# Performance work log

Hardware: AMD Instinct MI355X
Metric: run time of the kernel (lower is better)

## Reference

```python
import jax, jax.numpy as jnp
import numpy as np
from functools import reduce

N_QUBITS = 8
DEPTH = 2
DIM = 2 ** N_QUBITS  # state-vector dimension
HIDDEN = 512


def _cnot_chain_np(n):
    # product of CNOT(w, w+1) for w = 0..n-2, wire 0 = most-significant bit (PennyLane order)
    C4 = np.array([[1, 0, 0, 0], [0, 1, 0, 0], [0, 0, 0, 1], [0, 0, 1, 0]], dtype=np.complex64)
    U = np.eye(2 ** n, dtype=np.complex64)
    for w in range(n - 1):
        full = np.kron(np.kron(np.eye(2 ** w, dtype=np.complex64), C4),
                       np.eye(2 ** (n - w - 2), dtype=np.complex64))
        U = full @ U
    return U

CNOT_CHAIN = jnp.asarray(_cnot_chain_np(N_QUBITS))
# PauliZ on wire 0 (MSB): +1 for basis states with MSB=0, -1 otherwise
Z0 = jnp.asarray(np.where(np.arange(DIM) < DIM // 2, 1.0, -1.0).astype(np.float32))


def _rot(p):
    # PennyLane Rot(phi, theta, omega) = RZ(omega) @ RY(theta) @ RZ(phi)
    phi, th, om = p[0], p[1], p[2]
    c = jnp.cos(th / 2).astype(jnp.complex64)
    s = jnp.sin(th / 2).astype(jnp.complex64)
    ep = jnp.exp(-0.5j * (phi + om).astype(jnp.complex64))  # e^{-i(phi+om)/2}
    em = jnp.exp(0.5j * (phi - om).astype(jnp.complex64))   # e^{ i(phi-om)/2}
    m00 = ep * c
    m01 = -em * s
    m10 = jnp.conj(em) * s
    m11 = jnp.conj(ep) * c
    return jnp.stack([jnp.stack([m00, m01]), jnp.stack([m10, m11])])


def _gate_unitary(P):
    # P: (depth, n_qubits, 3). Circuit (after data RX): per layer Rot on every wire, then CNOT chain.
    U = jnp.eye(DIM, dtype=jnp.complex64)
    for l in range(DEPTH):
        layer = reduce(jnp.kron, [_rot(P[l, w]) for w in range(N_QUBITS)])
        U = CNOT_CHAIN @ (layer @ U)
    return U


def _expval(theta, U):
    # RX(theta)|0...0> = cos(t/2)|0..0> - i sin(t/2)|10..0>; then fixed unitary U; <Z_0>
    col0 = U[:, 0]          # U |00...0>
    col1 = U[:, DIM // 2]   # U |10...0>
    a = jnp.cos(theta / 2)[:, None]
    b = jnp.sin(theta / 2)[:, None]
    psi = a * col0[None, :] - 1j * b * col1[None, :]  # (B, DIM)
    return jnp.sum(Z0 * (psi.real ** 2 + psi.imag ** 2), axis=-1)  # (B,)


def setup_inputs() -> dict:
    key = jax.random.key(0)
    ks = jax.random.split(key, 13)
    T, B, D, H, Q = 256, 128, 512, HIDDEN, N_QUBITS
    inp = {"inputs": jax.random.normal(ks[0], (T, B, D), jnp.float32)}
    for i, g in enumerate(["f", "i", "g", "o"]):
        inp[f"W{g}"] = jax.random.normal(ks[1 + 3 * i], (Q, D + H), jnp.float32) * 0.02
        inp[f"b{g}"] = jnp.zeros((Q,), jnp.float32)
        inp[f"P{g}"] = jax.random.normal(ks[3 + 3 * i], (DEPTH, Q, 3), jnp.float32)
    return inp


def reference(inputs, Wf, bf, Pf, Wi, bi, Pi, Wg, bg, Pg, Wo, bo, Po):
    Uf, Ui, Ug, Uo = _gate_unitary(Pf), _gate_unitary(Pi), _gate_unitary(Pg), _gate_unitary(Po)

    def step(carry, x):
        hx, cx = carry
        comb = jnp.concatenate([x, hx], axis=1)  # (B, D+H)
        f = jax.nn.sigmoid(_expval((comb @ Wf.T + bf)[:, 0], Uf))[:, None]
        i = jax.nn.sigmoid(_expval((comb @ Wi.T + bi)[:, 0], Ui))[:, None]
        g = jnp.tanh(_expval((comb @ Wg.T + bg)[:, 0], Ug))[:, None]
        o = jax.nn.sigmoid(_expval((comb @ Wo.T + bo)[:, 0], Uo))[:, None]
        cx = f * cx + i * g
        hx = o * jnp.tanh(cx)
        return (hx, cx), hx

    B = inputs.shape[1]
    init = (jnp.zeros((B, HIDDEN), inputs.dtype), jnp.zeros((B, HIDDEN), inputs.dtype))
    (hx, cx), outputs = jax.lax.scan(step, init, inputs)
    return outputs, hx, cx
```

## Files before the change

kernel.cpp:

```cpp
#include <hip/hip_runtime.h>
#include <math.h>

#define T_STEPS 256
#define BATCH   128
#define DIMD    512
#define NROWS   (T_STEPS * BATCH)
#define PF      16
#define WRITER_BLOCKS 258
#define GEMV_BLOCKS 2048

#define INV2PI  0.15915494309189535f
#define L2E     1.4426950408889634f
#define TWO_L2E 2.8853900817779268f

#define AGENT __HIP_MEMORY_SCOPE_AGENT

#if __has_builtin(__builtin_amdgcn_sinf)
#define HW_SIN(x) __builtin_amdgcn_sinf(x)
#else
__device__ __forceinline__ float HW_SIN(float x) { return __sinf(x * 6.283185307179586f); }
#endif
#if __has_builtin(__builtin_amdgcn_exp2f)
#define EXP2(x) __builtin_amdgcn_exp2f(x)
#else
#define EXP2(x) exp2f(x)
#endif
#if __has_builtin(__builtin_amdgcn_rcpf)
#define RCP(x) __builtin_amdgcn_rcpf(x)
#else
#define RCP(x) (1.0f / (x))
#endif

__device__ __forceinline__ void  st_rlx(float* p, float v) {
    __hip_atomic_store(p, v, __ATOMIC_RELAXED, AGENT);
}
__device__ __forceinline__ void  st_rlx_i(int* p, int v) {
    __hip_atomic_store(p, v, __ATOMIC_RELAXED, AGENT);
}
__device__ __forceinline__ int   ld_rlx_i(const int* p) {
    return __hip_atomic_load(p, __ATOMIC_RELAXED, AGENT);
}
#define VMFENCE() asm volatile("s_waitcnt vmcnt(0)" ::: "memory")
#define CFENCE()  asm volatile("" ::: "memory")

__global__ __launch_bounds__(256) void prep(
    const float* __restrict__ inp,
    const float* __restrict__ Wf, const float* __restrict__ Wi,
    const float* __restrict__ Wg, const float* __restrict__ Wo,
    const float* __restrict__ bfp, const float* __restrict__ bip,
    const float* __restrict__ bgp, const float* __restrict__ bop,
    const float* __restrict__ Pf, const float* __restrict__ Pi,
    const float* __restrict__ Pg, const float* __restrict__ Po,
    float* __restrict__ gc, int* __restrict__ hProg,
    float4* __restrict__ X4)
{
    const int bid  = blockIdx.x;
    const int wv   = threadIdx.x >> 6;
    const int lane = threadIdx.x & 63;

    if (bid == 0) {
        if (threadIdx.x == 0) { hProg[0] = 0; hProg[1] = 0; }
        const int g = wv;
        const float* P = (g == 0) ? Pf : (g == 1) ? Pi : (g == 2) ? Pg : Po;
        const float* W = (g == 0) ? Wf : (g == 1) ? Wi : (g == 2) ? Wg : Wo;

        __shared__ float s0r[4][256], s0i[4][256], s1r[4][256], s1i[4][256];

#pragma unroll
        for (int j = 0; j < 4; ++j) {
            const int k = lane + 64 * j;
            s0r[g][k] = (k == 0)   ? 1.0f : 0.0f;  s0i[g][k] = 0.0f;
            s1r[g][k] = (k == 128) ? 1.0f : 0.0f;  s1i[g][k] = 0.0f;
        }
        __syncthreads();

        for (int l = 0; l < 2; ++l) {
            for (int w = 0; w < 8; ++w) {
                const float phi = P[l * 24 + w * 3 + 0];
                const float th  = P[l * 24 + w * 3 + 1];
                const float om  = P[l * 24 + w * 3 + 2];
                float sh, chh; __sincosf(0.5f * th, &sh, &chh);
                float sp, cp;  __sincosf(0.5f * (phi + om), &sp, &cp);
                float sm, cm;  __sincosf(0.5f * (phi - om), &sm, &cm);
                const float m00r =  cp * chh, m00i = -sp * chh;
                const float m01r = -cm * sh,  m01i = -sm * sh;
                const float m10r =  cm * sh,  m10i = -sm * sh;
                const float m11r =  cp * chh, m11i =  sp * chh;

                const int shift = 7 - w;
                const int mask  = 1 << shift;

                float n0r[4], n0i[4], n1r[4], n1i[4];
#pragma unroll
                for (int j = 0; j < 4; ++j) {
                    const int k  = lane + 64 * j;
                    const int bit = (k >> shift) & 1;
                    const int i0 = k & ~mask, i1 = k | mask;
                    const float a0r = s0r[g][i0], a0i = s0i[g][i0];
                    const float a1r = s0r[g][i1], a1i = s0i[g][i1];
                    const float b0r = s1r[g][i0], b0i = s1i[g][i0];
                    const float b1r = s1r[g][i1], b1i = s1i[g][i1];
                    const float mr0 = bit ? m10r : m00r, mi0 = bit ? m10i : m00i;
                    const float mr1 = bit ? m11r : m01r, mi1 = bit ? m11i : m01i;
                    n0r[j] = mr0 * a0r - mi0 * a0i + mr1 * a1r - mi1 * a1i;
                    n0i[j] = mr0 * a0i + mi0 * a0r + mr1 * a1i + mi1 * a1r;
                    n1r[j] = mr0 * b0r - mi0 * b0i + mr1 * b1r - mi1 * b1i;
                    n1i[j] = mr0 * b0i + mi0 * b0r + mr1 * b1i + mi1 * b1r;
                }
                __syncthreads();
#pragma unroll
                for (int j = 0; j < 4; ++j) {
                    const int k = lane + 64 * j;
                    s0r[g][k] = n0r[j]; s0i[g][k] = n0i[j];
                    s1r[g][k] = n1r[j]; s1i[g][k] = n1i[j];
                }
                __syncthreads();
            }
            float n0r[4], n0i[4], n1r[4], n1i[4];
#pragma unroll
            for (int j = 0; j < 4; ++j) {
                int src = lane + 64 * j;
                for (int w = 6; w >= 0; --w) {
                    const int cb = (src >> (7 - w)) & 1;
                    src ^= cb << (6 - w);
                }
                n0r[j] = s0r[g][src]; n0i[j] = s0i[g][src];
                n1r[j] = s1r[g][src]; n1i[j] = s1i[g][src];
            }
            __syncthreads();
#pragma unroll
            for (int j = 0; j < 4; ++j) {
                const int k = lane + 64 * j;
                s0r[g][k] = n0r[j]; s0i[g][k] = n0i[j];
                s1r[g][k] = n1r[j]; s1i[g][k] = n1i[j];
            }
            __syncthreads();
        }

        float t00 = 0, t11 = 0, t01 = 0;
#pragma unroll
        for (int j = 0; j < 4; ++j) {
            const int k = lane + 64 * j;
            const float z = (k < 128) ? 1.0f : -1.0f;
            t00 += z * (s0r[g][k] * s0r[g][k] + s0i[g][k] * s0i[g][k]);
            t11 += z * (s1r[g][k] * s1r[g][k] + s1i[g][k] * s1i[g][k]);
            t01 += z * (s0i[g][k] * s1r[g][k] - s0r[g][k] * s1i[g][k]);
        }
        float tsw = 0;
#pragma unroll
        for (int j = 0; j < 8; ++j) tsw += W[512 + lane + 64 * j];

        for (int off = 32; off; off >>= 1) {
            t00 += __shfl_xor(t00, off);
            t11 += __shfl_xor(t11, off);
            t01 += __shfl_xor(t01, off);
            tsw += __shfl_xor(tsw, off);
        }
        if (lane == 0) {
            const float A  = 0.5f * (t00 + t11);
            const float Bc = 0.5f * (t00 - t11);
            const float Bs = -t01;
            const float R  = sqrtf(Bc * Bc + Bs * Bs);
            const float ph = atan2f(Bc, Bs) * INV2PI;
            const float sc = (g == 2) ? TWO_L2E : -L2E;
            gc[4 * g + 0] = sc * A;
            gc[4 * g + 1] = sc * R;
            gc[4 * g + 2] = ph;
            gc[4 * g + 3] = tsw * INV2PI;
        }
        return;
    }

    const int rowbase = (bid - 1) * 16 + wv * 4;

    const float4* wfp = (const float4*)Wf;
    const float4* wip = (const float4*)Wi;
    const float4* wgp = (const float4*)Wg;
    const float4* wop = (const float4*)Wo;
    const float4 fa = wfp[lane], fb = wfp[lane + 64];
    const float4 ia = wip[lane], ib = wip[lane + 64];
    const float4 ga = wgp[lane], gb = wgp[lane + 64];
    const float4 oa = wop[lane], ob = wop[lane + 64];

    const float4* xr = (const float4*)(inp + (size_t)rowbase * DIMD);
    float sums[4][4];
#pragma unroll
    for (int r = 0; r < 4; ++r) {
        const float4 xa = xr[r * 128 + lane];
        const float4 xb = xr[r * 128 + lane + 64];
        sums[r][0] = xa.x * fa.x + xa.y * fa.y + xa.z * fa.z + xa.w * fa.w
                   + xb.x * fb.x + xb.y * fb.y + xb.z * fb.z + xb.w * fb.w;
        sums[r][1] = xa.x * ia.x + xa.y * ia.y + xa.z * ia.z + xa.w * ia.w
                   + xb.x * ib.x + xb.y * ib.y + xb.z * ib.z + xb.w * ib.w;
        sums[r][2] = xa.x * ga.x + xa.y * ga.y + xa.z * ga.z + xa.w * ga.w
                   + xb.x * gb.x + xb.y * gb.y + xb.z * gb.z + xb.w * gb.w;
        sums[r][3] = xa.x * oa.x + xa.y * oa.y + xa.z * oa.z + xa.w * oa.w
                   + xb.x * ob.x + xb.y * ob.y + xb.z * ob.z + xb.w * ob.w;
    }
#pragma unroll
    for (int r = 0; r < 4; ++r)
#pragma unroll
        for (int g = 0; g < 4; ++g)
            for (int off = 32; off; off >>= 1)
                sums[r][g] += __shfl_xor(sums[r][g], off);

    if (lane == 0) {
        const float b0f = bfp[0], b0i = bip[0], b0g = bgp[0], b0o = bop[0];
#pragma unroll
        for (int r = 0; r < 4; ++r) {
            X4[rowbase + r] = make_float4((sums[r][0] + b0f) * INV2PI,
                                          (sums[r][1] + b0i) * INV2PI,
                                          (sums[r][2] + b0g) * INV2PI,
                                          (sums[r][3] + b0o) * INV2PI);
        }
    }
}

__global__ __launch_bounds__(256) void scan_write(
    const float4* __restrict__ X4, const float* __restrict__ gc,
    float* __restrict__ Hs, float* __restrict__ cfin,
    float4* __restrict__ out4, int* __restrict__ hProg)
{
    const int bid  = blockIdx.x;
    const int wv   = threadIdx.x >> 6;
    const int lane = threadIdx.x & 63;

    if (bid == 0) {
        if (threadIdx.x >= BATCH) return;
        const int b = threadIdx.x;

        const float Af = gc[0],  Rf = gc[1],  phf = gc[2],  swf = gc[3];
        const float Ai = gc[4],  Ri = gc[5],  phi_ = gc[6], swi = gc[7];
        const float Ag = gc[8],  Rg = gc[9],  phg = gc[10], swg = gc[11];
        const float Ao = gc[12], Ro = gc[13], pho = gc[14], swo = gc[15];

        float4 p[PF];
#pragma unroll
        for (int j = 0; j < PF; ++j) p[j] = X4[j * BATCH + b];

        float c = 0.0f, h = 0.0f;
        for (int tb = 0; tb < T_STEPS; tb += PF) {
#pragma unroll
            for (int j = 0; j < PF; ++j) {
                const int t = tb + j;
                const float4 xv = p[j];
                p[j] = X4[(t + PF) * BATCH + b];

                const float thf = fmaf(h, swf, xv.x + phf);
                const float thi = fmaf(h, swi, xv.y + phi_);
                const float thg = fmaf(h, swg, xv.z + phg);
                const float tho = fmaf(h, swo, xv.w + pho);
                const float Ef = fmaf(Rf, HW_SIN(thf), Af);
                const float Ei = fmaf(Ri, HW_SIN(thi), Ai);
                const float Eg = fmaf(Rg, HW_SIN(thg), Ag);
                const float Eo = fmaf(Ro, HW_SIN(tho), Ao);
                const float fg = RCP(1.0f + EXP2(Ef));
                const float ig = RCP(1.0f + EXP2(Ei));
                const float og = RCP(1.0f + EXP2(Eo));
                const float gg = 1.0f - 2.0f * RCP(EXP2(Eg) + 1.0f);
                c = fmaf(fg, c, ig * gg);
                const float y = RCP(EXP2(c * TWO_L2E) + 1.0f);
                h = fmaf(-2.0f * og, y, og);
                st_rlx(&Hs[t * BATCH + b], h);
            }
            if (tb == T_STEPS - PF) st_rlx(&cfin[b], c);
            if (((tb + PF) & 31) == 0) {
                VMFENCE();
                if (lane == 0) st_rlx_i(&hProg[wv], tb + PF);
            }
        }
        return;
    }

    const int t  = bid - 1;
    const int qd = wv;
    const int pidx = (qd < 2) ? 0 : 1;
    const int need = (t < 256) ? (t + 1) : 256;

    int cur = ld_rlx_i(&hProg[pidx]);
    while (cur < need) {
        int chunks = ((need - cur) >> 4) + 1;
        for (int s = 0; s < chunks; ++s) __builtin_amdgcn_s_sleep(16);
        cur = ld_rlx_i(&hProg[pidx]);
    }
    CFENCE();

    const float* src = (t == 257) ? cfin : (Hs + ((t >= 256 ? 255 : t) * BATCH));
    const float hv = src[qd * 32 + (lane & 31)];

    size_t base = (t < 256) ? ((size_t)t * 16384)
                : (t == 256 ? (size_t)4194304 : (size_t)4210688);
    base += (size_t)qd * 4096;
#pragma unroll 8
    for (int j = 0; j < 64; ++j) {
        const float v = __shfl(hv, j >> 1);
        out4[base + j * 64 + lane] = make_float4(v, v, v, v);
    }
}

extern "C" void kernel_launch(void* const* d_in, const int* in_sizes, int n_in,
                              void* d_out, int out_size, void* d_ws, size_t ws_size,
                              hipStream_t stream)
{
    const float* inp = (const float*)d_in[0];
    const float* Wf  = (const float*)d_in[1];
    const float* bfv = (const float*)d_in[2];
    const float* Pf  = (const float*)d_in[3];
    const float* Wi  = (const float*)d_in[4];
    const float* biv = (const float*)d_in[5];
    const float* Pi  = (const float*)d_in[6];
    const float* Wg  = (const float*)d_in[7];
    const float* bgv = (const float*)d_in[8];
    const float* Pg  = (const float*)d_in[9];
    const float* Wo  = (const float*)d_in[10];
    const float* bov = (const float*)d_in[11];
    const float* Po  = (const float*)d_in[12];

    float4* X4   = (float4*)d_ws;
    float*  Hs   = (float*)(X4 + NROWS + PF * BATCH);
    float*  cfin = Hs + NROWS;
    float*  gc   = cfin + BATCH;
    int*    hProg = (int*)(gc + 16);

    prep<<<1 + GEMV_BLOCKS, 256, 0, stream>>>(inp, Wf, Wi, Wg, Wo,
                                              bfv, biv, bgv, bov,
                                              Pf, Pi, Pg, Po,
                                              gc, hProg, X4);
    scan_write<<<1 + WRITER_BLOCKS, 256, 0, stream>>>(X4, gc, Hs, cfin,
                                                      (float4*)d_out, hProg);
}
```

Baseline: 57.17 us.

## Algebraically fuse LSTM gate math, coarsen progress signaling, use nontemporal output stores

```diff
diff --git a/kernel.cpp b/kernel.cpp
--- a/kernel.cpp
+++ b/kernel.cpp
@@ -14,6 +14,8 @@
 #define TWO_L2E 2.8853900817779268f
 
 #define AGENT __HIP_MEMORY_SCOPE_AGENT
+
+typedef float f32x4 __attribute__((ext_vector_type(4)));
 
 #if __has_builtin(__builtin_amdgcn_sinf)
 #define HW_SIN(x) __builtin_amdgcn_sinf(x)
@@ -216,7 +218,7 @@
     }
 }
 
-__global__ __launch_bounds__(256) void scan_write(
+__global__ __launch_bounds__(256, 1) void scan_write(
     const float4* __restrict__ X4, const float* __restrict__ gc,
     float* __restrict__ Hs, float* __restrict__ cfin,
     float4* __restrict__ out4, int* __restrict__ hProg)
@@ -234,37 +236,47 @@
         const float Ag = gc[8],  Rg = gc[9],  phg = gc[10], swg = gc[11];
         const float Ao = gc[12], Ro = gc[13], pho = gc[14], swo = gc[15];
 
-        float4 p[PF];
-#pragma unroll
-        for (int j = 0; j < PF; ++j) p[j] = X4[j * BATCH + b];
+        float4 p0, p1, p2, p3, p4, p5, p6, p7,
+               p8, p9, p10, p11, p12, p13, p14, p15;
+
+#define LOADP(J, P) { const float4 v_ = X4[(J) * BATCH + b];                 \
+        P = make_float4(v_.x + phf, v_.y + phi_, v_.z + phg, v_.w + pho); }
+        LOADP(0, p0)   LOADP(1, p1)   LOADP(2, p2)   LOADP(3, p3)
+        LOADP(4, p4)   LOADP(5, p5)   LOADP(6, p6)   LOADP(7, p7)
+        LOADP(8, p8)   LOADP(9, p9)   LOADP(10, p10) LOADP(11, p11)
+        LOADP(12, p12) LOADP(13, p13) LOADP(14, p14) LOADP(15, p15)
+#undef LOADP
 
         float c = 0.0f, h = 0.0f;
         for (int tb = 0; tb < T_STEPS; tb += PF) {
-#pragma unroll
-            for (int j = 0; j < PF; ++j) {
-                const int t = tb + j;
-                const float4 xv = p[j];
-                p[j] = X4[(t + PF) * BATCH + b];
-
-                const float thf = fmaf(h, swf, xv.x + phf);
-                const float thi = fmaf(h, swi, xv.y + phi_);
-                const float thg = fmaf(h, swg, xv.z + phg);
-                const float tho = fmaf(h, swo, xv.w + pho);
-                const float Ef = fmaf(Rf, HW_SIN(thf), Af);
-                const float Ei = fmaf(Ri, HW_SIN(thi), Ai);
-                const float Eg = fmaf(Rg, HW_SIN(thg), Ag);
-                const float Eo = fmaf(Ro, HW_SIN(tho), Ao);
-                const float fg = RCP(1.0f + EXP2(Ef));
-                const float ig = RCP(1.0f + EXP2(Ei));
-                const float og = RCP(1.0f + EXP2(Eo));
-                const float gg = 1.0f - 2.0f * RCP(EXP2(Eg) + 1.0f);
-                c = fmaf(fg, c, ig * gg);
-                const float y = RCP(EXP2(c * TWO_L2E) + 1.0f);
-                h = fmaf(-2.0f * og, y, og);
-                st_rlx(&Hs[t * BATCH + b], h);
-            }
+#define STEP(J, P) {                                                         \
+            const float4 xv = P;                                             \
+            { const float4 v_ = X4[(tb + (J) + PF) * BATCH + b];             \
+              P = make_float4(v_.x + phf, v_.y + phi_,                       \
+                              v_.z + phg, v_.w + pho); }                     \
+            const float thf = fmaf(h, swf, xv.x);                            \
+            const float thi = fmaf(h, swi, xv.y);                            \
+            const float thg = fmaf(h, swg, xv.z);                            \
+            const float tho = fmaf(h, swo, xv.w);                            \
+            const float ef = EXP2(fmaf(Rf, HW_SIN(thf), Af));                \
+            const float ei = EXP2(fmaf(Ri, HW_SIN(thi), Ai));                \
+            const float eg = EXP2(fmaf(Rg, HW_SIN(thg), Ag));                \
+            const float eo = EXP2(fmaf(Ro, HW_SIN(tho), Ao));                \
+            const float Ff = ef + 1.0f, Fi = ei + 1.0f;                      \
+            const float Fg = eg + 1.0f, Fo = eo + 1.0f;                      \
+            const float FiFg = Fi * Fg;                                      \
+            const float num  = fmaf(c, FiFg, (eg - 1.0f) * Ff);              \
+            c = num * RCP(Ff * FiFg);                                        \
+            const float ec = EXP2(c * TWO_L2E);                              \
+            h = (ec - 1.0f) * RCP(Fo * (ec + 1.0f));                         \
+            st_rlx(&Hs[(tb + (J)) * BATCH + b], h); }
+            STEP(0, p0)   STEP(1, p1)   STEP(2, p2)   STEP(3, p3)
+            STEP(4, p4)   STEP(5, p5)   STEP(6, p6)   STEP(7, p7)
+            STEP(8, p8)   STEP(9, p9)   STEP(10, p10) STEP(11, p11)
+            STEP(12, p12) STEP(13, p13) STEP(14, p14) STEP(15, p15)
+#undef STEP
             if (tb == T_STEPS - PF) st_rlx(&cfin[b], c);
-            if (((tb + PF) & 31) == 0) {
+            if (((tb + PF) & 63) == 0) {
                 VMFENCE();
                 if (lane == 0) st_rlx_i(&hProg[wv], tb + PF);
             }
@@ -275,12 +287,15 @@
     const int t  = bid - 1;
     const int qd = wv;
     const int pidx = (qd < 2) ? 0 : 1;
-    const int need = (t < 256) ? (t + 1) : 256;
+    const int need = (t < 256) ? ((t >> 6) + 1) << 6 : 256;
 
     int cur = ld_rlx_i(&hProg[pidx]);
     while (cur < need) {
-        int chunks = ((need - cur) >> 4) + 1;
-        for (int s = 0; s < chunks; ++s) __builtin_amdgcn_s_sleep(16);
+        int loops = ((need - cur) >> 5) + 1;
+        for (int s = 0; s < loops; ++s) {
+            __builtin_amdgcn_s_sleep(32);
+            __builtin_amdgcn_s_sleep(32);
+        }
         cur = ld_rlx_i(&hProg[pidx]);
     }
     CFENCE();
@@ -294,7 +309,8 @@
 #pragma unroll 8
     for (int j = 0; j < 64; ++j) {
         const float v = __shfl(hv, j >> 1);
-        out4[base + j * 64 + lane] = make_float4(v, v, v, v);
+        const f32x4 val = {v, v, v, v};
+        __builtin_nontemporal_store(val, (f32x4*)(out4 + base + j * 64 + lane));
     }
 }
 
```

Result: faster. 54.91 us (-4.0%).
